# Kernel tuning notes

Measured on AMD Instinct MI355X. Metric: run time of the kernel, lower is better.

The kernel has to match this reference:

```python
import jax, jax.numpy as jnp
import numpy as np

N = 100000   # nodes
E = 1600000  # edges
F_IN = 4
H = 64
G = 1000     # graphs in batch
C = 3        # num_classes
L = 2        # num_unit (LEConv layers)


def setup_inputs() -> dict:
    key = jax.random.key(0)
    ks = jax.random.split(key, 14)
    s = 0.1
    return {
        "x": jax.random.normal(ks[0], (N, F_IN), jnp.float32),
        "edge_index": jax.random.randint(ks[1], (2, E), 0, N, dtype=jnp.int32),
        "edge_attr": jax.random.uniform(ks[2], (E,), jnp.float32),
        "batch": jnp.sort(jax.random.randint(ks[3], (N,), 0, G, dtype=jnp.int32)),
        "w_emb": jax.random.normal(ks[4], (F_IN, H), jnp.float32) * s,
        "b_emb": jnp.zeros((H,), jnp.float32),
        "lin1_w": jax.random.normal(ks[5], (L, H, H), jnp.float32) * s,
        "lin1_b": jnp.zeros((L, H), jnp.float32),
        "lin2_w": jax.random.normal(ks[6], (L, H, H), jnp.float32) * s,  # bias=False in PyG LEConv
        "lin3_w": jax.random.normal(ks[7], (L, H, H), jnp.float32) * s,
        "lin3_b": jnp.zeros((L, H), jnp.float32),
        "mlp_w1": jax.random.normal(ks[8], (H, 2 * H), jnp.float32) * s,
        "mlp_b1": jnp.zeros((2 * H,), jnp.float32),
        "mlp_w2": jax.random.normal(ks[9], (2 * H, C), jnp.float32) * s,
        "mlp_b2": jnp.zeros((C,), jnp.float32),
    }


def reference(x, edge_index, edge_attr, batch, w_emb, b_emb,
              lin1_w, lin1_b, lin2_w, lin3_w, lin3_b,
              mlp_w1, mlp_b1, mlp_w2, mlp_b2):
    src, dst = edge_index[0], edge_index[1]  # message flows src(j) -> dst(i)
    h = x @ w_emb + b_emb  # [N, H]
    for l in range(L):
        a = h @ lin1_w[l] + lin1_b[l]            # lin1(x_j) source side
        b = h @ lin2_w[l]                         # lin2(x_i) target side, no bias
        msg = (a[src] - b[dst]) * edge_attr[:, None]   # [E, H]
        agg = jax.ops.segment_sum(msg, dst, num_segments=N)
        h = jax.nn.relu(agg + h @ lin3_w[l] + lin3_b[l])
    # global_mean_pool
    sums = jax.ops.segment_sum(h, batch, num_segments=G)        # [G, H]
    counts = jax.ops.segment_sum(jnp.ones((N,), h.dtype), batch, num_segments=G)
    graph_x = sums / jnp.maximum(counts, 1.0)[:, None]
    # causal_mlp head
    return jax.nn.relu(graph_x @ mlp_w1 + mlp_b1) @ mlp_w2 + mlp_b2  # [G, C]
```

## Files before the change

kernel.cpp:

```cpp
#include <hip/hip_runtime.h>

#define N_NODES 100000
#define N_EDGES 1600000
#define F_INPUT 4
#define HDIM 64
#define G_GRAPHS 1000
#define C_CLS 3

#define NPB 256
#define BSHIFT 8
#define NB 391
#define CBLK 391
#define CSR_CAP 6144
#define EMB_BLOCKS 25000
#define HIST_BLOCKS 512

typedef __attribute__((ext_vector_type(8))) short bf16x8;
typedef __attribute__((ext_vector_type(4))) float f32x4;

__device__ __forceinline__ unsigned short f2bf(float f) {
    unsigned u = __float_as_uint(f);
    unsigned r = (u + 0x7FFF + ((u >> 16) & 1)) >> 16;
    return (unsigned short)r;
}
__device__ __forceinline__ float bflo(unsigned u) {
    return __uint_as_float(u << 16);
}
__device__ __forceinline__ float bfhi(unsigned u) {
    return __uint_as_float(u & 0xFFFF0000u);
}

__global__ __launch_bounds__(256) void k_emb_hist(
    const float* __restrict__ x, const float* __restrict__ w, const float* __restrict__ b,
    float* __restrict__ h, const int* __restrict__ dst, int* __restrict__ bcnt) {
    __shared__ int s[NB];
    if (blockIdx.x < EMB_BLOCKS) {
        int t = blockIdx.x * 256 + threadIdx.x;
        if (t >= N_NODES * HDIM) return;
        int n = t >> 6, f = t & 63;
        const float* xr = x + n * F_INPUT;
        float acc = b[f];
#pragma unroll
        for (int k = 0; k < F_INPUT; ++k) acc += xr[k] * w[k * HDIM + f];
        h[t] = acc;
    } else {
        int bb = blockIdx.x - EMB_BLOCKS;
        for (int i = threadIdx.x; i < NB; i += 256) s[i] = 0;
        __syncthreads();
        for (int e = bb * 256 + threadIdx.x; e < N_EDGES; e += HIST_BLOCKS * 256)
            atomicAdd(&s[dst[e] >> BSHIFT], 1);
        __syncthreads();
        for (int i = threadIdx.x; i < NB; i += 256)
            if (s[i]) atomicAdd(&bcnt[i], s[i]);
    }
}

__global__ __launch_bounds__(512) void k_boff_bounds(
    const int* __restrict__ bcnt, int* __restrict__ boff, int* __restrict__ bcur,
    const int* __restrict__ batch, int* __restrict__ goff) {
    if (blockIdx.x == 0) {
        __shared__ int s[512];
        int t = threadIdx.x;
        int v = (t < NB) ? bcnt[t] : 0;
        s[t] = v;
        __syncthreads();
        for (int d = 1; d < 512; d <<= 1) {
            int x2 = (t >= d) ? s[t - d] : 0;
            __syncthreads();
            s[t] += x2;
            __syncthreads();
        }
        int ex = s[t] - v;
        if (t < NB) { boff[t] = ex; bcur[t] = ex; }
        if (t == 0) boff[NB] = N_EDGES;
    } else {
        int n = (blockIdx.x - 1) * 512 + threadIdx.x;
        if (n >= N_NODES) return;
        int bv = batch[n];
        int bp = (n == 0) ? -1 : batch[n - 1];
        for (int g = bp + 1; g <= bv; ++g) goff[g] = n;
        if (n == N_NODES - 1) {
            for (int g = bv + 1; g <= G_GRAPHS; ++g) goff[g] = N_NODES;
        }
    }
}

__global__ __launch_bounds__(1024) void k_bucket(const int* __restrict__ src,
                                                 const int* __restrict__ dst,
                                                 const float* __restrict__ attr,
                                                 int* __restrict__ bcur,
                                                 int2* __restrict__ bbuf) {
    __shared__ int cnt[NB];
    __shared__ int base[NB];
    for (int i = threadIdx.x; i < NB; i += 1024) cnt[i] = 0;
    __syncthreads();
    int e0 = blockIdx.x * 4096;
    int myb[4], myrank[4];
    int2 mypack[4];
#pragma unroll
    for (int k = 0; k < 4; ++k) {
        int e = e0 + k * 1024 + threadIdx.x;
        if (e < N_EDGES) {
            int d = dst[e];
            int b = d >> BSHIFT;
            myb[k] = b;
            myrank[k] = atomicAdd(&cnt[b], 1);
            mypack[k].x = src[e] | ((d & (NPB - 1)) << 17);
            mypack[k].y = __float_as_int(attr[e]);
        } else
            myb[k] = -1;
    }
    __syncthreads();
    for (int i = threadIdx.x; i < NB; i += 1024)
        base[i] = cnt[i] ? atomicAdd(&bcur[i], cnt[i]) : 0;
    __syncthreads();
#pragma unroll
    for (int k = 0; k < 4; ++k)
        if (myb[k] >= 0) bbuf[base[myb[k]] + myrank[k]] = mypack[k];
}

__global__ __launch_bounds__(256) void k_csr(const int2* __restrict__ bbuf,
                                             const int* __restrict__ boff,
                                             int* __restrict__ off,
                                             float* __restrict__ wsum,
                                             int2* __restrict__ edge2) {
    __shared__ int2 se[CSR_CAP];
    __shared__ int deg[NPB];
    __shared__ float wsm[NPB];
    __shared__ int loff[NPB];
    __shared__ int sct[256];
    int b = blockIdx.x;
    int lo = boff[b];
    int cnt = boff[b + 1] - lo;
    if (cnt > CSR_CAP) cnt = CSR_CAP;
    int t = threadIdx.x;
    deg[t] = 0;
    wsm[t] = 0.f;
    for (int i = t; i < cnt; i += 256) se[i] = bbuf[lo + i];
    __syncthreads();
    for (int i = t; i < cnt; i += 256) {
        int2 p = se[i];
        int dloc = (p.x >> 17) & (NPB - 1);
        atomicAdd(&deg[dloc], 1);
        atomicAdd(&wsm[dloc], __int_as_float(p.y));
    }
    __syncthreads();
    int v = deg[t];
    sct[t] = v;
    __syncthreads();
    for (int d = 1; d < 256; d <<= 1) {
        int x2 = (t >= d) ? sct[t - d] : 0;
        __syncthreads();
        sct[t] += x2;
        __syncthreads();
    }
    int ex = sct[t] - v;
    loff[t] = ex;
    __syncthreads();
    int n = b * NPB + t;
    if (n < N_NODES) { off[n] = lo + ex; wsum[n] = wsm[t]; }
    if (b == NB - 1 && t == 0) off[N_NODES] = N_EDGES;
    deg[t] = 0;
    __syncthreads();
    for (int i = t; i < cnt; i += 256) {
        int2 p = se[i];
        int dloc = (p.x >> 17) & (NPB - 1);
        int r = atomicAdd(&deg[dloc], 1);
        edge2[lo + loff[dloc] + r] = make_int2(p.x & 0x1FFFF, p.y);
    }
}

__global__ __launch_bounds__(256) void k_gemm3(
    const float* __restrict__ h,
    const float* __restrict__ W1, const float* __restrict__ b1,
    const float* __restrict__ W2,
    const float* __restrict__ W3, const float* __restrict__ b3,
    const float* __restrict__ wsum,
    unsigned short* __restrict__ a_out, float* __restrict__ d_out_) {
    int wave = threadIdx.x >> 6;
    int lane = threadIdx.x & 63;
    int row = lane & 15;
    int kg = lane >> 4;
    int base = blockIdx.x * 64;
    int col = wave * 16 + row;

    bf16x8 Bf[3][2];
    const float* Ws[3] = {W1, W2, W3};
#pragma unroll
    for (int m = 0; m < 3; ++m)
#pragma unroll
        for (int hf = 0; hf < 2; ++hf) {
            union { bf16x8 v; unsigned short u[8]; } fr;
#pragma unroll
            for (int j = 0; j < 8; ++j) {
                int k = hf * 32 + kg * 8 + j;
                fr.u[j] = f2bf(Ws[m][k * HDIM + col]);
            }
            Bf[m][hf] = fr.v;
        }

    float bias1 = b1[col];
    float bias3 = b3[col];

    f32x4 acc[3][4];
#pragma unroll
    for (int m = 0; m < 3; ++m)
#pragma unroll
        for (int t = 0; t < 4; ++t) acc[m][t] = (f32x4){0.f, 0.f, 0.f, 0.f};

#pragma unroll
    for (int t = 0; t < 4; ++t) {
        int n = base + t * 16 + row;
        union { bf16x8 v; unsigned short u[8]; } a0, a1;
        if (n < N_NODES) {
            const float* hr = h + (size_t)n * HDIM;
            float4 p0 = *(const float4*)(hr + kg * 8);
            float4 p1 = *(const float4*)(hr + kg * 8 + 4);
            float4 q0 = *(const float4*)(hr + 32 + kg * 8);
            float4 q1 = *(const float4*)(hr + 32 + kg * 8 + 4);
            a0.u[0] = f2bf(p0.x); a0.u[1] = f2bf(p0.y); a0.u[2] = f2bf(p0.z); a0.u[3] = f2bf(p0.w);
            a0.u[4] = f2bf(p1.x); a0.u[5] = f2bf(p1.y); a0.u[6] = f2bf(p1.z); a0.u[7] = f2bf(p1.w);
            a1.u[0] = f2bf(q0.x); a1.u[1] = f2bf(q0.y); a1.u[2] = f2bf(q0.z); a1.u[3] = f2bf(q0.w);
            a1.u[4] = f2bf(q1.x); a1.u[5] = f2bf(q1.y); a1.u[6] = f2bf(q1.z); a1.u[7] = f2bf(q1.w);
        } else {
#pragma unroll
            for (int j = 0; j < 8; ++j) { a0.u[j] = 0; a1.u[j] = 0; }
        }
#pragma unroll
        for (int m = 0; m < 3; ++m) {
            acc[m][t] = __builtin_amdgcn_mfma_f32_16x16x32_bf16(a0.v, Bf[m][0], acc[m][t], 0, 0, 0);
            acc[m][t] = __builtin_amdgcn_mfma_f32_16x16x32_bf16(a1.v, Bf[m][1], acc[m][t], 0, 0, 0);
        }
    }

#pragma unroll
    for (int t = 0; t < 4; ++t) {
#pragma unroll
        for (int r = 0; r < 4; ++r) {
            int n = base + t * 16 + kg * 4 + r;
            if (n >= N_NODES) continue;
            float ws = wsum[n];
            float av = acc[0][t][r] + bias1;
            float dv = acc[2][t][r] + bias3 - acc[1][t][r] * ws;
            a_out[(size_t)n * HDIM + col] = f2bf(av);
            d_out_[(size_t)n * HDIM + col] = dv;
        }
    }
}

__global__ __launch_bounds__(256) void k_agg(const int2* __restrict__ edge2,
                                             const int* __restrict__ off,
                                             const unsigned short* __restrict__ a,
                                             const float* __restrict__ dbuf,
                                             float* __restrict__ h) {
    int wid = threadIdx.x >> 6;
    int lane = threadIdx.x & 63;
    int slot = lane >> 3;
    int fo = lane & 7;
    int n = blockIdx.x * 4 + wid;
    if (n >= N_NODES) return;
    int lo = off[n], hi = off[n + 1];

    float acc[8];
#pragma unroll
    for (int q = 0; q < 8; ++q) acc[q] = 0.f;

    for (int j0 = lo; j0 < hi; j0 += 16) {
        int j1 = j0 + slot;
        int j2 = j0 + 8 + slot;
        if (j1 < hi) {
            int2 p = edge2[j1];
            float w = __int_as_float(p.y);
            uint4 u = *(const uint4*)(a + (size_t)p.x * HDIM + fo * 8);
            acc[0] += bflo(u.x) * w; acc[1] += bfhi(u.x) * w;
            acc[2] += bflo(u.y) * w; acc[3] += bfhi(u.y) * w;
            acc[4] += bflo(u.z) * w; acc[5] += bfhi(u.z) * w;
            acc[6] += bflo(u.w) * w; acc[7] += bfhi(u.w) * w;
        }
        if (j2 < hi) {
            int2 p = edge2[j2];
            float w = __int_as_float(p.y);
            uint4 u = *(const uint4*)(a + (size_t)p.x * HDIM + fo * 8);
            acc[0] += bflo(u.x) * w; acc[1] += bfhi(u.x) * w;
            acc[2] += bflo(u.y) * w; acc[3] += bfhi(u.y) * w;
            acc[4] += bflo(u.z) * w; acc[5] += bfhi(u.z) * w;
            acc[6] += bflo(u.w) * w; acc[7] += bfhi(u.w) * w;
        }
    }

#pragma unroll
    for (int m = 8; m <= 32; m <<= 1) {
#pragma unroll
        for (int q = 0; q < 8; ++q) acc[q] += __shfl_xor(acc[q], m);
    }

    if (slot == 0) {
        size_t o = (size_t)n * HDIM + fo * 8;
        float4 d0 = *(const float4*)(dbuf + o);
        float4 d1 = *(const float4*)(dbuf + o + 4);
        float4 o0, o1;
        o0.x = fmaxf(acc[0] + d0.x, 0.f); o0.y = fmaxf(acc[1] + d0.y, 0.f);
        o0.z = fmaxf(acc[2] + d0.z, 0.f); o0.w = fmaxf(acc[3] + d0.w, 0.f);
        o1.x = fmaxf(acc[4] + d1.x, 0.f); o1.y = fmaxf(acc[5] + d1.y, 0.f);
        o1.z = fmaxf(acc[6] + d1.z, 0.f); o1.w = fmaxf(acc[7] + d1.w, 0.f);
        *(float4*)(h + o) = o0;
        *(float4*)(h + o + 4) = o1;
    }
}

__global__ __launch_bounds__(128) void k_poolhead(const float* __restrict__ h,
                                                  const int* __restrict__ goff,
                                                  const float* __restrict__ W1,
                                                  const float* __restrict__ b1,
                                                  const float* __restrict__ W2,
                                                  const float* __restrict__ b2,
                                                  float* __restrict__ out) {
    int g = blockIdx.x;
    __shared__ float part[128];
    __shared__ float sx[HDIM];
    __shared__ float sy[2 * HDIM];
    int t = threadIdx.x;
    int lo = goff[g], hi = goff[g + 1];
    int f = t & 63, half = t >> 6;
    float acc = 0.f;
    for (int n = lo + half; n < hi; n += 2) acc += h[(size_t)n * HDIM + f];
    part[t] = acc;
    __syncthreads();
    if (t < HDIM) sx[t] = (part[t] + part[t + 64]) / fmaxf((float)(hi - lo), 1.f);
    __syncthreads();
    float a1 = b1[t];
    for (int k = 0; k < HDIM; ++k) a1 += sx[k] * W1[k * 2 * HDIM + t];
    sy[t] = fmaxf(a1, 0.f);
    __syncthreads();
    if (t < C_CLS) {
        float o = b2[t];
        for (int k = 0; k < 2 * HDIM; ++k) o += sy[k] * W2[k * C_CLS + t];
        out[g * C_CLS + t] = o;
    }
}

extern "C" void kernel_launch(void* const* d_in, const int* in_sizes, int n_in,
                              void* d_out, int out_size, void* d_ws, size_t ws_size,
                              hipStream_t stream) {
    const float* x      = (const float*)d_in[0];
    const int*   ei     = (const int*)d_in[1];
    const float* eattr  = (const float*)d_in[2];
    const int*   batch  = (const int*)d_in[3];
    const float* w_emb  = (const float*)d_in[4];
    const float* b_emb  = (const float*)d_in[5];
    const float* lin1_w = (const float*)d_in[6];
    const float* lin1_b = (const float*)d_in[7];
    const float* lin2_w = (const float*)d_in[8];
    const float* lin3_w = (const float*)d_in[9];
    const float* lin3_b = (const float*)d_in[10];
    const float* mlp_w1 = (const float*)d_in[11];
    const float* mlp_b1 = (const float*)d_in[12];
    const float* mlp_w2 = (const float*)d_in[13];
    const float* mlp_b2 = (const float*)d_in[14];
    float* out = (float*)d_out;

    const int* src = ei;
    const int* dst = ei + N_EDGES;

    const size_t NH = (size_t)N_NODES * HDIM;
    float* fws = (float*)d_ws;
    float* h    = fws;
    float* dbuf = h + NH;
    float* wsum = dbuf + NH;
    unsigned short* abf = (unsigned short*)(wsum + N_NODES);
    int2* edge2 = (int2*)(abf + NH);
    int2* bbuf  = edge2 + N_EDGES;
    int* off    = (int*)(bbuf + N_EDGES);
    int* bcnt   = off + N_NODES + 1;
    int* bcur   = bcnt + NB;
    int* boff   = bcur + NB;
    int* goff   = boff + NB + 1;

    hipMemsetAsync(bcnt, 0, NB * sizeof(int), stream);

    k_emb_hist<<<EMB_BLOCKS + HIST_BLOCKS, 256, 0, stream>>>(x, w_emb, b_emb, h, dst, bcnt);
    k_boff_bounds<<<1 + (N_NODES + 511) / 512, 512, 0, stream>>>(bcnt, boff, bcur, batch, goff);
    k_bucket<<<CBLK, 1024, 0, stream>>>(src, dst, eattr, bcur, bbuf);
    k_csr<<<NB, 256, 0, stream>>>(bbuf, boff, off, wsum, edge2);

    int gemm_blocks = (N_NODES + 63) / 64;
    int agg_blocks = (N_NODES + 3) / 4;

    for (int l = 0; l < 2; ++l) {
        const float* W1 = lin1_w + l * HDIM * HDIM;
        const float* B1 = lin1_b + l * HDIM;
        const float* W2 = lin2_w + l * HDIM * HDIM;
        const float* W3 = lin3_w + l * HDIM * HDIM;
        const float* B3 = lin3_b + l * HDIM;
        k_gemm3<<<gemm_blocks, 256, 0, stream>>>(h, W1, B1, W2, W3, B3, wsum, abf, dbuf);
        k_agg<<<agg_blocks, 256, 0, stream>>>(edge2, off, abf, dbuf, h);
    }

    k_poolhead<<<G_GRAPHS, 128, 0, stream>>>(h, goff, mlp_w1, mlp_b1, mlp_w2, mlp_b2, out);
}
```

Measured before the change: 263.0 us.

## Store node features and self-term buffer in bf16 across all kernels

Switches the hidden-state buffer h and the per-node self-term buffer from fp32 to bf16 storage throughout embedding, GEMM, aggregation and pooling. This halves their memory traffic, and the GEMM can now load bf16 fragments directly instead of converting on load. The embedding kernel now writes four features per thread, and the bucket kernel processes 8192 edges per block with half as many blocks. The cost is an extra bf16 rounding of intermediate activations between layers, which adds numerical error.

```diff
diff --git a/kernel.cpp b/kernel.cpp
--- a/kernel.cpp
+++ b/kernel.cpp
@@ -10,9 +10,9 @@
 #define NPB 256
 #define BSHIFT 8
 #define NB 391
-#define CBLK 391
+#define CBLK 196
 #define CSR_CAP 6144
-#define EMB_BLOCKS 25000
+#define EMB_BLOCKS 6250
 #define HIST_BLOCKS 512
 
 typedef __attribute__((ext_vector_type(8))) short bf16x8;
@@ -29,20 +29,28 @@
 __device__ __forceinline__ float bfhi(unsigned u) {
     return __uint_as_float(u & 0xFFFF0000u);
 }
+__device__ __forceinline__ float bf1(unsigned short s) {
+    return __uint_as_float(((unsigned)s) << 16);
+}
 
 __global__ __launch_bounds__(256) void k_emb_hist(
     const float* __restrict__ x, const float* __restrict__ w, const float* __restrict__ b,
-    float* __restrict__ h, const int* __restrict__ dst, int* __restrict__ bcnt) {
+    unsigned short* __restrict__ h, const int* __restrict__ dst, int* __restrict__ bcnt) {
     __shared__ int s[NB];
     if (blockIdx.x < EMB_BLOCKS) {
         int t = blockIdx.x * 256 + threadIdx.x;
-        if (t >= N_NODES * HDIM) return;
-        int n = t >> 6, f = t & 63;
+        int n = t >> 4, f0 = (t & 15) * 4;
         const float* xr = x + n * F_INPUT;
-        float acc = b[f];
-#pragma unroll
-        for (int k = 0; k < F_INPUT; ++k) acc += xr[k] * w[k * HDIM + f];
-        h[t] = acc;
+        float x0 = xr[0], x1 = xr[1], x2 = xr[2], x3 = xr[3];
+        ushort4 o;
+        {
+            float a0 = b[f0+0] + x0*w[0*HDIM+f0+0] + x1*w[1*HDIM+f0+0] + x2*w[2*HDIM+f0+0] + x3*w[3*HDIM+f0+0];
+            float a1 = b[f0+1] + x0*w[0*HDIM+f0+1] + x1*w[1*HDIM+f0+1] + x2*w[2*HDIM+f0+1] + x3*w[3*HDIM+f0+1];
+            float a2 = b[f0+2] + x0*w[0*HDIM+f0+2] + x1*w[1*HDIM+f0+2] + x2*w[2*HDIM+f0+2] + x3*w[3*HDIM+f0+2];
+            float a3 = b[f0+3] + x0*w[0*HDIM+f0+3] + x1*w[1*HDIM+f0+3] + x2*w[2*HDIM+f0+3] + x3*w[3*HDIM+f0+3];
+            o.x = f2bf(a0); o.y = f2bf(a1); o.z = f2bf(a2); o.w = f2bf(a3);
+        }
+        *(ushort4*)(h + (size_t)n * HDIM + f0) = o;
     } else {
         int bb = blockIdx.x - EMB_BLOCKS;
         for (int i = threadIdx.x; i < NB; i += 256) s[i] = 0;
@@ -94,11 +102,11 @@
     __shared__ int base[NB];
     for (int i = threadIdx.x; i < NB; i += 1024) cnt[i] = 0;
     __syncthreads();
-    int e0 = blockIdx.x * 4096;
-    int myb[4], myrank[4];
-    int2 mypack[4];
-#pragma unroll
-    for (int k = 0; k < 4; ++k) {
+    int e0 = blockIdx.x * 8192;
+    int myb[8], myrank[8];
+    int2 mypack[8];
+#pragma unroll
+    for (int k = 0; k < 8; ++k) {
         int e = e0 + k * 1024 + threadIdx.x;
         if (e < N_EDGES) {
             int d = dst[e];
@@ -115,7 +123,7 @@
         base[i] = cnt[i] ? atomicAdd(&bcur[i], cnt[i]) : 0;
     __syncthreads();
 #pragma unroll
-    for (int k = 0; k < 4; ++k)
+    for (int k = 0; k < 8; ++k)
         if (myb[k] >= 0) bbuf[base[myb[k]] + myrank[k]] = mypack[k];
 }
 
@@ -171,12 +179,12 @@
 }
 
 __global__ __launch_bounds__(256) void k_gemm3(
-    const float* __restrict__ h,
+    const unsigned short* __restrict__ h,
     const float* __restrict__ W1, const float* __restrict__ b1,
     const float* __restrict__ W2,
     const float* __restrict__ W3, const float* __restrict__ b3,
     const float* __restrict__ wsum,
-    unsigned short* __restrict__ a_out, float* __restrict__ d_out_) {
+    unsigned short* __restrict__ a_out, unsigned short* __restrict__ d_out_) {
     int wave = threadIdx.x >> 6;
     int lane = threadIdx.x & 63;
     int row = lane & 15;
@@ -211,25 +219,19 @@
 #pragma unroll
     for (int t = 0; t < 4; ++t) {
         int n = base + t * 16 + row;
-        union { bf16x8 v; unsigned short u[8]; } a0, a1;
+        bf16x8 a0, a1;
         if (n < N_NODES) {
-            const float* hr = h + (size_t)n * HDIM;
-            float4 p0 = *(const float4*)(hr + kg * 8);
-            float4 p1 = *(const float4*)(hr + kg * 8 + 4);
-            float4 q0 = *(const float4*)(hr + 32 + kg * 8);
-            float4 q1 = *(const float4*)(hr + 32 + kg * 8 + 4);
-            a0.u[0] = f2bf(p0.x); a0.u[1] = f2bf(p0.y); a0.u[2] = f2bf(p0.z); a0.u[3] = f2bf(p0.w);
-            a0.u[4] = f2bf(p1.x); a0.u[5] = f2bf(p1.y); a0.u[6] = f2bf(p1.z); a0.u[7] = f2bf(p1.w);
-            a1.u[0] = f2bf(q0.x); a1.u[1] = f2bf(q0.y); a1.u[2] = f2bf(q0.z); a1.u[3] = f2bf(q0.w);
-            a1.u[4] = f2bf(q1.x); a1.u[5] = f2bf(q1.y); a1.u[6] = f2bf(q1.z); a1.u[7] = f2bf(q1.w);
+            const unsigned short* hr = h + (size_t)n * HDIM;
+            a0 = *(const bf16x8*)(hr + kg * 8);
+            a1 = *(const bf16x8*)(hr + 32 + kg * 8);
         } else {
-#pragma unroll
-            for (int j = 0; j < 8; ++j) { a0.u[j] = 0; a1.u[j] = 0; }
+            a0 = (bf16x8){0,0,0,0,0,0,0,0};
+            a1 = (bf16x8){0,0,0,0,0,0,0,0};
         }
 #pragma unroll
         for (int m = 0; m < 3; ++m) {
-            acc[m][t] = __builtin_amdgcn_mfma_f32_16x16x32_bf16(a0.v, Bf[m][0], acc[m][t], 0, 0, 0);
-            acc[m][t] = __builtin_amdgcn_mfma_f32_16x16x32_bf16(a1.v, Bf[m][1], acc[m][t], 0, 0, 0);
+            acc[m][t] = __builtin_amdgcn_mfma_f32_16x16x32_bf16(a0, Bf[m][0], acc[m][t], 0, 0, 0);
+            acc[m][t] = __builtin_amdgcn_mfma_f32_16x16x32_bf16(a1, Bf[m][1], acc[m][t], 0, 0, 0);
         }
     }
 
@@ -243,7 +245,7 @@
             float av = acc[0][t][r] + bias1;
             float dv = acc[2][t][r] + bias3 - acc[1][t][r] * ws;
             a_out[(size_t)n * HDIM + col] = f2bf(av);
-            d_out_[(size_t)n * HDIM + col] = dv;
+            d_out_[(size_t)n * HDIM + col] = f2bf(dv);
         }
     }
 }
@@ -251,8 +253,8 @@
 __global__ __launch_bounds__(256) void k_agg(const int2* __restrict__ edge2,
                                              const int* __restrict__ off,
                                              const unsigned short* __restrict__ a,
-                                             const float* __restrict__ dbuf,
-                                             float* __restrict__ h) {
+                                             const unsigned short* __restrict__ dbuf,
+                                             unsigned short* __restrict__ h) {
     int wid = threadIdx.x >> 6;
     int lane = threadIdx.x & 63;
     int slot = lane >> 3;
@@ -296,19 +298,21 @@
 
     if (slot == 0) {
         size_t o = (size_t)n * HDIM + fo * 8;
-        float4 d0 = *(const float4*)(dbuf + o);
-        float4 d1 = *(const float4*)(dbuf + o + 4);
-        float4 o0, o1;
-        o0.x = fmaxf(acc[0] + d0.x, 0.f); o0.y = fmaxf(acc[1] + d0.y, 0.f);
-        o0.z = fmaxf(acc[2] + d0.z, 0.f); o0.w = fmaxf(acc[3] + d0.w, 0.f);
-        o1.x = fmaxf(acc[4] + d1.x, 0.f); o1.y = fmaxf(acc[5] + d1.y, 0.f);
-        o1.z = fmaxf(acc[6] + d1.z, 0.f); o1.w = fmaxf(acc[7] + d1.w, 0.f);
-        *(float4*)(h + o) = o0;
-        *(float4*)(h + o + 4) = o1;
-    }
-}
-
-__global__ __launch_bounds__(128) void k_poolhead(const float* __restrict__ h,
+        uint4 dv = *(const uint4*)(dbuf + o);
+        float dd[8] = {bflo(dv.x), bfhi(dv.x), bflo(dv.y), bfhi(dv.y),
+                       bflo(dv.z), bfhi(dv.z), bflo(dv.w), bfhi(dv.w)};
+        unsigned r[4];
+#pragma unroll
+        for (int q = 0; q < 4; ++q) {
+            unsigned lo16 = f2bf(fmaxf(acc[2 * q] + dd[2 * q], 0.f));
+            unsigned hi16 = f2bf(fmaxf(acc[2 * q + 1] + dd[2 * q + 1], 0.f));
+            r[q] = lo16 | (hi16 << 16);
+        }
+        *(uint4*)(h + o) = make_uint4(r[0], r[1], r[2], r[3]);
+    }
+}
+
+__global__ __launch_bounds__(128) void k_poolhead(const unsigned short* __restrict__ h,
                                                   const int* __restrict__ goff,
                                                   const float* __restrict__ W1,
                                                   const float* __restrict__ b1,
@@ -323,7 +327,7 @@
     int lo = goff[g], hi = goff[g + 1];
     int f = t & 63, half = t >> 6;
     float acc = 0.f;
-    for (int n = lo + half; n < hi; n += 2) acc += h[(size_t)n * HDIM + f];
+    for (int n = lo + half; n < hi; n += 2) acc += bf1(h[(size_t)n * HDIM + f]);
     part[t] = acc;
     __syncthreads();
     if (t < HDIM) sx[t] = (part[t] + part[t + 64]) / fmaxf((float)(hi - lo), 1.f);
@@ -363,12 +367,11 @@
     const int* dst = ei + N_EDGES;
 
     const size_t NH = (size_t)N_NODES * HDIM;
-    float* fws = (float*)d_ws;
-    float* h    = fws;
-    float* dbuf = h + NH;
-    float* wsum = dbuf + NH;
-    unsigned short* abf = (unsigned short*)(wsum + N_NODES);
-    int2* edge2 = (int2*)(abf + NH);
+    unsigned short* h   = (unsigned short*)d_ws;
+    unsigned short* dbf = h + NH;
+    unsigned short* abf = dbf + NH;
+    float* wsum = (float*)(abf + NH);
+    int2* edge2 = (int2*)(wsum + N_NODES);
     int2* bbuf  = edge2 + N_EDGES;
     int* off    = (int*)(bbuf + N_EDGES);
     int* bcnt   = off + N_NODES + 1;
@@ -392,8 +395,8 @@
         const float* W2 = lin2_w + l * HDIM * HDIM;
         const float* W3 = lin3_w + l * HDIM * HDIM;
         const float* B3 = lin3_b + l * HDIM;
-        k_gemm3<<<gemm_blocks, 256, 0, stream>>>(h, W1, B1, W2, W3, B3, wsum, abf, dbuf);
-        k_agg<<<agg_blocks, 256, 0, stream>>>(edge2, off, abf, dbuf, h);
+        k_gemm3<<<gemm_blocks, 256, 0, stream>>>(h, W1, B1, W2, W3, B3, wsum, abf, dbf);
+        k_agg<<<agg_blocks, 256, 0, stream>>>(edge2, off, abf, dbf, h);
     }
 
     k_poolhead<<<G_GRAPHS, 128, 0, stream>>>(h, goff, mlp_w1, mlp_b1, mlp_w2, mlp_b2, out);
```

Result: faster. 240.2 us (-8.6%).
